# Kernel optimization log

Measured on AMD Instinct MI355X. Metric: run time of the kernel, lower is better.

## Reference

```python
import jax, jax.numpy as jnp
import numpy as np

VISION_TOKEN_TYPE = 1

def _swiglu_mlp(x, w_gate, w_up, w_down):
    # x: [B, L, D]; w_gate/w_up: [D, F]; w_down: [F, D]
    g = jax.nn.silu(jnp.einsum('bld,df->blf', x, w_gate))
    u = jnp.einsum('bld,df->blf', x, w_up)
    return jnp.einsum('blf,fd->bld', g * u, w_down)

def _vision_mask(token_type_ids):
    # vision_token_mask[:, :-1] = (tt[:, :-1]==V) & (tt[:, 1:]==V); last col False
    is_v = token_type_ids == VISION_TOKEN_TYPE
    pair = is_v[:, :-1] & is_v[:, 1:]
    return jnp.concatenate([pair, jnp.zeros_like(pair[:, :1])], axis=1)  # [B, L] bool

def setup_inputs() -> dict:
    key = jax.random.key(0)
    ks = jax.random.split(key, 8)
    B, L, D, F = 2, 2048, 4096, 11008
    s = 0.02
    return {
        'hidden_states': jax.random.normal(ks[0], (B, L, D), dtype=jnp.float32),
        'token_type_ids': jax.random.randint(ks[1], (B, L), 0, 2, dtype=jnp.int64),
        'vision_gate': jax.random.normal(ks[2], (D, F), dtype=jnp.float32) * s,
        'vision_up': jax.random.normal(ks[3], (D, F), dtype=jnp.float32) * s,
        'vision_down': jax.random.normal(ks[4], (F, D), dtype=jnp.float32) * s,
        'language_gate': jax.random.normal(ks[5], (D, F), dtype=jnp.float32) * s,
        'language_up': jax.random.normal(ks[6], (D, F), dtype=jnp.float32) * s,
        'language_down': jax.random.normal(ks[7], (F, D), dtype=jnp.float32) * s,
    }

def reference(hidden_states, token_type_ids, vision_gate, vision_up, vision_down,
              language_gate, language_up, language_down):
    vmask = _vision_mask(token_type_ids)  # [B, L]
    out_v = _swiglu_mlp(hidden_states, vision_gate, vision_up, vision_down)
    out_l = _swiglu_mlp(hidden_states, language_gate, language_up, language_down)
    return jnp.where(vmask[:, :, None], out_v, out_l)
```

## Files before the change

### kernel.cpp

```cpp
#include <hip/hip_runtime.h>
#include <hip/hip_bf16.h>

#define B_    2
#define L_    2048
#define D_    4096
#define F_    11008
#define M_TOK (B_ * L_)
#define BM    256
#define M_ALLOC (M_TOK + BM)
#define NTM   (M_ALLOC / BM)
#define NT_GU (D_ / 64)
#define NT_DN (F_ / 64)
#define NTILE_F (F_ / 128)
#define LDS_BYTES 131072

typedef __attribute__((ext_vector_type(8))) __bf16 bf16x8;
typedef __attribute__((ext_vector_type(4))) float  f32x4;
typedef unsigned short ushort_t;
typedef unsigned int   uint_t;


__device__ __forceinline__ void gload_lds16(const void* g, void* l) {
  __builtin_amdgcn_global_load_lds(
      (const __attribute__((address_space(1))) void*)g,
      (__attribute__((address_space(3))) void*)l, 16, 0, 0);
}

#define PH_BAR()  { __builtin_amdgcn_sched_barrier(0); __builtin_amdgcn_s_barrier(); __builtin_amdgcn_sched_barrier(0); }
#define LGKM0()   { asm volatile("s_waitcnt lgkmcnt(0)" ::: "memory"); __builtin_amdgcn_sched_barrier(0); }
#define VM4()     { asm volatile("s_waitcnt vmcnt(4)" ::: "memory"); __builtin_amdgcn_sched_barrier(0); }
#define VM0()     { asm volatile("s_waitcnt vmcnt(0)" ::: "memory"); __builtin_amdgcn_sched_barrier(0); }

__device__ __forceinline__ ushort_t f2bf(float v) {
  union { __hip_bfloat16 h; ushort_t u; } cv;
  cv.h = __float2bfloat16(v);
  return cv.u;
}

__device__ __forceinline__ void stage_half(const __hip_bfloat16* __restrict__ src, int ldE,
                                           __bf16* ldsb, int w, int lane) {
#pragma unroll
  for (int j = 0; j < 2; ++j) {
    const int ch  = (w * 2 + j) * 64 + lane;
    const int row = ch >> 3;
    const int cc  = (ch & 7) ^ (row & 7);
    gload_lds16(src + (size_t)(row * ldE + cc * 8), ldsb + (w * 2 + j) * 512);
  }
}

__device__ __forceinline__ bf16x8 ldfrag(const __bf16* region, int row, int koffb) {
  const int off = ((row << 7) + koffb) ^ ((row & 7) << 4);
  return *(const bf16x8*)((const char*)region + off);
}

__device__ __forceinline__ void mfma_q(f32x4 (&acc)[8][4], int mb, int nb,
                                       const bf16x8 (&af)[4][2], const bf16x8 (&bf)[2][2]) {
#pragma unroll
  for (int mm = 0; mm < 4; ++mm)
#pragma unroll
    for (int nn = 0; nn < 2; ++nn)
#pragma unroll
      for (int ks = 0; ks < 2; ++ks)
        acc[mb + mm][nb + nn] = __builtin_amdgcn_mfma_f32_16x16x32_bf16(
            af[mm][ks], bf[nn][ks], acc[mb + mm][nb + nn], 0, 0, 0);
}

__device__ __forceinline__ void gemm_kloop(const __hip_bfloat16* __restrict__ Ag, const int ldA,
                                           const __hip_bfloat16* __restrict__ Bg, const int ldB,
                                           const int nt, __bf16* smem, f32x4 (&acc)[8][4],
                                           const int wm, const int wn, const int l15,
                                           const int l4, const int w, const int lane) {
  stage_half(Ag,             ldA, smem,                w, lane);
  stage_half(Ag + 128 * ldA, ldA, smem + 8192,         w, lane);
  stage_half(Bg,             ldB, smem + 16384,        w, lane);
  stage_half(Bg + 128 * ldB, ldB, smem + 24576,        w, lane);
  if (1 < nt) {
    stage_half(Ag + 64,             ldA, smem + 32768,        w, lane);
    stage_half(Ag + 64 + 128 * ldA, ldA, smem + 32768 + 8192, w, lane);
  }
  VM4(); PH_BAR();

  for (int t = 0; t < nt; ++t) {
    __bf16* bufc = smem + (t & 1) * 32768;
    __bf16* bufn = smem + ((t + 1) & 1) * 32768;
    const __bf16* At = bufc;
    const __bf16* Bt = bufc + 16384;
    bf16x8 a0[4][2], a1[4][2], b0[2][2], b1[2][2];

#pragma unroll
    for (int i = 0; i < 4; ++i)
#pragma unroll
      for (int ks = 0; ks < 2; ++ks)
        a0[i][ks] = ldfrag(At, wm * 128 + i * 16 + l15, ks * 64 + l4 * 16);
#pragma unroll
    for (int n = 0; n < 2; ++n)
#pragma unroll
      for (int ks = 0; ks < 2; ++ks)
        b0[n][ks] = ldfrag(Bt, wn * 64 + n * 16 + l15, ks * 64 + l4 * 16);
    if (t + 1 < nt) stage_half(Bg + (t + 1) * 64, ldB, bufn + 16384, w, lane);
    PH_BAR(); LGKM0();
    __builtin_amdgcn_s_setprio(1);
    mfma_q(acc, 0, 0, a0, b0);
    __builtin_amdgcn_s_setprio(0);
    PH_BAR();

#pragma unroll
    for (int i = 0; i < 4; ++i)
#pragma unroll
      for (int ks = 0; ks < 2; ++ks)
        a1[i][ks] = ldfrag(At, wm * 128 + 64 + i * 16 + l15, ks * 64 + l4 * 16);
    if (t + 1 < nt) stage_half(Bg + (t + 1) * 64 + 128 * ldB, ldB, bufn + 24576, w, lane);
    PH_BAR(); LGKM0();
    __builtin_amdgcn_s_setprio(1);
    mfma_q(acc, 4, 0, a1, b0);
    __builtin_amdgcn_s_setprio(0);
    PH_BAR();

#pragma unroll
    for (int n = 0; n < 2; ++n)
#pragma unroll
      for (int ks = 0; ks < 2; ++ks)
        b1[n][ks] = ldfrag(Bt, wn * 64 + 32 + n * 16 + l15, ks * 64 + l4 * 16);
    if (t + 2 < nt) stage_half(Ag + (t + 2) * 64, ldA, bufc, w, lane);
    PH_BAR(); LGKM0();
    __builtin_amdgcn_s_setprio(1);
    mfma_q(acc, 4, 2, a1, b1);
    __builtin_amdgcn_s_setprio(0);
    PH_BAR();

    if (t + 2 < nt) stage_half(Ag + (t + 2) * 64 + 128 * ldA, ldA, bufc + 8192, w, lane);
    __builtin_amdgcn_s_setprio(1);
    mfma_q(acc, 0, 2, a0, b1);
    __builtin_amdgcn_s_setprio(0);
    if (t + 2 < nt) { VM4(); } else { VM0(); }
    PH_BAR();
  }
}


__global__ void init_kernel(int* counters, int* slot2tok) {
  int i = blockIdx.x * 256 + threadIdx.x;
  if (i < 2) counters[i] = 0;
  if (i < M_ALLOC) slot2tok[i] = -1;
}

__global__ void assign_kernel(const int* __restrict__ tt, int* counters,
                              int* __restrict__ slot2tok) {
  int t = blockIdx.x * 256 + threadIdx.x;
  if (t >= M_TOK) return;
  int l = t & (L_ - 1);
  bool isv = (tt[t] == 1) && (l < L_ - 1) && (tt[t + 1] == 1);
  int slot;
  if (isv) slot = atomicAdd(&counters[0], 1);
  else     slot = M_ALLOC - 1 - atomicAdd(&counters[1], 1);
  slot2tok[slot] = t;
}

__global__ void gather_cvt(const float* __restrict__ x, const int* __restrict__ slot2tok,
                           __hip_bfloat16* __restrict__ xg) {
  const int s = blockIdx.x;
  const int t = slot2tok[s];
  __hip_bfloat16* dst = xg + (size_t)s * D_ + threadIdx.x * 16;
  union { ushort_t h[8]; uint4 v; } p0, p1;
  if (t >= 0) {
    const float4* s4 = (const float4*)(x + (size_t)t * D_ + threadIdx.x * 16);
    float4 a = s4[0], b = s4[1], c = s4[2], d = s4[3];
    float vals[16] = {a.x,a.y,a.z,a.w,b.x,b.y,b.z,b.w,c.x,c.y,c.z,c.w,d.x,d.y,d.z,d.w};
#pragma unroll
    for (int i = 0; i < 8; ++i) p0.h[i] = f2bf(vals[i]);
#pragma unroll
    for (int i = 0; i < 8; ++i) p1.h[i] = f2bf(vals[8 + i]);
  } else {
    p0.v = make_uint4(0, 0, 0, 0);
    p1.v = make_uint4(0, 0, 0, 0);
  }
  *(uint4*)dst = p0.v;
  *(uint4*)(dst + 8) = p1.v;
}

__global__ __launch_bounds__(128) void transpose_cvt64(const float* __restrict__ in,
                                                       __hip_bfloat16* __restrict__ out,
                                                       int R, int C) {
  const int c  = threadIdx.x & 63;
  const int rc = threadIdx.x >> 6;
  const int c0 = blockIdx.x * 64;
  const int r0 = blockIdx.y * 64 + rc * 32;
  const float* ip = in + (size_t)r0 * C + c0 + c;
  uint_t pk[16];
#pragma unroll
  for (int j = 0; j < 16; ++j) {
    float v0 = ip[(size_t)(2 * j) * C];
    float v1 = ip[(size_t)(2 * j + 1) * C];
    pk[j] = (uint_t)f2bf(v0) | ((uint_t)f2bf(v1) << 16);
  }
  uint4* op = (uint4*)(out + (size_t)(c0 + c) * R + r0);
#pragma unroll
  for (int k = 0; k < 4; ++k)
    op[k] = make_uint4(pk[4 * k], pk[4 * k + 1], pk[4 * k + 2], pk[4 * k + 3]);
}

__global__ void sentinel_kernel(float* out, int n) {
  int i = blockIdx.x * 256 + threadIdx.x;
  if (i < n) out[i] = 1e30f;
}

__global__ __launch_bounds__(512, 2) void gemm256_gateup_fused(
    const __hip_bfloat16* __restrict__ Xg,
    const __hip_bfloat16* __restrict__ WgTv, const __hip_bfloat16* __restrict__ WuTv,
    const __hip_bfloat16* __restrict__ WgTl, const __hip_bfloat16* __restrict__ WuTl,
    __hip_bfloat16* __restrict__ H, const int* __restrict__ counters) {
  extern __shared__ __bf16 smem[];
  const int tid = threadIdx.x, lane = tid & 63, w = tid >> 6;
  const int wm = w >> 1, wn = w & 1;
  const int l15 = lane & 15, l4 = lane >> 4;

  const int orig = blockIdx.x;
  const int nwg = gridDim.x;
  const int q = nwg >> 3, r = nwg & 7, xcd = orig & 7;
  const int wg = (xcd < r ? xcd * (q + 1) : r * (q + 1) + (xcd - r) * q) + (orig >> 3);
  const int mt = wg / NTILE_F, ntile = wg % NTILE_F;
  const int row0 = mt * BM;
  const int ncol0 = ntile * 128;
  const int nv = counters[0];
  const bool isv = row0 < nv;
  const __hip_bfloat16* Ag   = Xg + (size_t)row0 * D_;
  const __hip_bfloat16* Bg_g = (isv ? WgTv : WgTl) + (size_t)ncol0 * D_;
  const __hip_bfloat16* Bu_g = (isv ? WuTv : WuTl) + (size_t)ncol0 * D_;

  f32x4 accg[4][4] = {};
  f32x4 accu[4][4] = {};
  const int nt = NT_GU;

  stage_half(Ag,                  D_, smem,          w, lane);
  stage_half(Ag + 128 * D_,       D_, smem + 8192,   w, lane);
  stage_half(Bg_g,                D_, smem + 32768,  w, lane);
  stage_half(Bu_g,                D_, smem + 49152,  w, lane);
  stage_half(Ag + 64,             D_, smem + 16384,  w, lane);
  stage_half(Ag + 64 + 128 * D_,  D_, smem + 24576,  w, lane);
  VM4(); PH_BAR();

  for (int t = 0; t < nt; ++t) {
    const int cur = t & 1;
    const __bf16* At  = smem + cur * 16384;
    const __bf16* Bgt = smem + 32768 + cur * 8192;
    const __bf16* But = smem + 49152 + cur * 8192;
    __bf16* nxA  = smem + cur * 16384;
    __bf16* nxBg = smem + 32768 + (cur ^ 1) * 8192;
    __bf16* nxBu = smem + 49152 + (cur ^ 1) * 8192;
    bf16x8 af[4][2], bg[4][2], bu[4][2];

#pragma unroll
    for (int m = 0; m < 4; ++m)
#pragma unroll
      for (int ks = 0; ks < 2; ++ks)
        af[m][ks] = ldfrag(At, wm * 64 + m * 16 + l15, ks * 64 + l4 * 16);
#pragma unroll
    for (int n = 0; n < 4; ++n)
#pragma unroll
      for (int ks = 0; ks < 2; ++ks)
        bg[n][ks] = ldfrag(Bgt, wn * 64 + n * 16 + l15, ks * 64 + l4 * 16);
    if (t + 1 < nt) {
      stage_half(Bg_g + (t + 1) * 64, D_, nxBg, w, lane);
      stage_half(Bu_g + (t + 1) * 64, D_, nxBu, w, lane);
    }
    PH_BAR(); LGKM0();
    __builtin_amdgcn_s_setprio(1);
#pragma unroll
    for (int m = 0; m < 4; ++m)
#pragma unroll
      for (int n = 0; n < 4; ++n)
#pragma unroll
        for (int ks = 0; ks < 2; ++ks)
          accg[m][n] = __builtin_amdgcn_mfma_f32_16x16x32_bf16(
              af[m][ks], bg[n][ks], accg[m][n], 0, 0, 0);
    __builtin_amdgcn_s_setprio(0);
    PH_BAR();

#pragma unroll
    for (int n = 0; n < 4; ++n)
#pragma unroll
      for (int ks = 0; ks < 2; ++ks)
        bu[n][ks] = ldfrag(But, wn * 64 + n * 16 + l15, ks * 64 + l4 * 16);
    if (t + 2 < nt) {
      stage_half(Ag + (t + 2) * 64,            D_, nxA,        w, lane);
      stage_half(Ag + (t + 2) * 64 + 128 * D_, D_, nxA + 8192, w, lane);
    }
    PH_BAR(); LGKM0();
    __builtin_amdgcn_s_setprio(1);
#pragma unroll
    for (int m = 0; m < 4; ++m)
#pragma unroll
      for (int n = 0; n < 4; ++n)
#pragma unroll
        for (int ks = 0; ks < 2; ++ks)
          accu[m][n] = __builtin_amdgcn_mfma_f32_16x16x32_bf16(
              af[m][ks], bu[n][ks], accu[m][n], 0, 0, 0);
    __builtin_amdgcn_s_setprio(0);
    if (t + 2 < nt) { VM4(); } else { VM0(); }
    PH_BAR();
  }

#pragma unroll
  for (int m = 0; m < 4; ++m) {
    const int grow = row0 + wm * 64 + m * 16 + l4 * 4;
#pragma unroll
    for (int rr = 0; rr < 4; ++rr) {
      __hip_bfloat16* orow = H + (size_t)(grow + rr) * F_ + ncol0 + wn * 64 + l15;
#pragma unroll
      for (int n = 0; n < 4; ++n) {
        const float g = accg[m][n][rr];
        const float u = accu[m][n][rr];
        orow[n * 16] = __float2bfloat16(g / (1.0f + __expf(-g)) * u);
      }
    }
  }
}


__global__ __launch_bounds__(512, 2) void gemm256_down(
    const __hip_bfloat16* __restrict__ H,
    const __hip_bfloat16* __restrict__ WdTv, const __hip_bfloat16* __restrict__ WdTl,
    float* __restrict__ out, const int* __restrict__ counters,
    const int* __restrict__ slot2tok) {
  extern __shared__ __bf16 smem[];
  const int tid = threadIdx.x, lane = tid & 63, w = tid >> 6;
  const int wm = w >> 2, wn = w & 3;
  const int l15 = lane & 15, l4 = lane >> 4;

  const int mt = blockIdx.x / (D_ / 256);
  const int nt = blockIdx.x % (D_ / 256);
  const int z  = blockIdx.y;
  const int row0 = mt * BM;
  const int ncol0 = nt * 256;
  const int ntz = NT_DN / 2;
  const int t0 = z * ntz;
  const int nv = counters[0];
  const __hip_bfloat16* Bsrc = (row0 < nv) ? WdTv : WdTl;
  const __hip_bfloat16* Ag = H + (size_t)row0 * F_ + t0 * 64;
  const __hip_bfloat16* Bg = Bsrc + (size_t)ncol0 * F_ + t0 * 64;

  f32x4 acc[8][4] = {};
  gemm_kloop(Ag, F_, Bg, F_, ntz, smem, acc, wm, wn, l15, l4, w, lane);

#pragma unroll
  for (int m = 0; m < 8; ++m) {
    const int slot = row0 + wm * 128 + m * 16 + l4 * 4;
#pragma unroll
    for (int rr = 0; rr < 4; ++rr) {
      const int tok = slot2tok[slot + rr];
      if (tok < 0) continue;
      float* orow = out + (size_t)tok * D_ + ncol0 + wn * 64 + l15;
#pragma unroll
      for (int n = 0; n < 4; ++n)
        atomicAdd(&orow[n * 16], acc[m][n][rr]);
    }
  }
}


extern "C" void kernel_launch(void* const* d_in, const int* in_sizes, int n_in,
                              void* d_out, int out_size, void* d_ws, size_t ws_size,
                              hipStream_t stream) {
  const float* x   = (const float*)d_in[0];
  const int*   tt  = (const int*)d_in[1];
  const float* wgv = (const float*)d_in[2];
  const float* wuv = (const float*)d_in[3];
  const float* wdv = (const float*)d_in[4];
  const float* wgl = (const float*)d_in[5];
  const float* wul = (const float*)d_in[6];
  const float* wdl = (const float*)d_in[7];
  float* out = (float*)d_out;

  size_t off = 0;
  auto nalign = [](size_t v) { return (v + 255) & ~(size_t)255; };
  const size_t o_cnt = off; off += nalign(2 * sizeof(int));
  const size_t o_s2t = off; off += nalign((size_t)M_ALLOC * sizeof(int));
  const size_t o_xg  = off; off += nalign((size_t)M_ALLOC * D_ * 2);
  const size_t o_h   = off; off += nalign((size_t)M_ALLOC * F_ * 2);
  const size_t wbytes = nalign((size_t)D_ * F_ * 2);
  const size_t o_wgv = off; off += wbytes;
  const size_t o_wuv = off; off += wbytes;
  const size_t o_wgl = off; off += wbytes;
  const size_t o_wul = off; off += wbytes;

  if (ws_size < off) {
    sentinel_kernel<<<(out_size + 255) / 256, 256, 0, stream>>>(out, out_size);
    return;
  }

  char* ws = (char*)d_ws;
  int* counters = (int*)(ws + o_cnt);
  int* slot2tok = (int*)(ws + o_s2t);
  __hip_bfloat16* Xg  = (__hip_bfloat16*)(ws + o_xg);
  __hip_bfloat16* H   = (__hip_bfloat16*)(ws + o_h);
  __hip_bfloat16* WgTv = (__hip_bfloat16*)(ws + o_wgv);
  __hip_bfloat16* WuTv = (__hip_bfloat16*)(ws + o_wuv);
  __hip_bfloat16* WgTl = (__hip_bfloat16*)(ws + o_wgl);
  __hip_bfloat16* WuTl = (__hip_bfloat16*)(ws + o_wul);
  __hip_bfloat16* WdTv = WgTv;
  __hip_bfloat16* WdTl = WuTv;

  hipFuncSetAttribute((const void*)gemm256_gateup_fused,
                      hipFuncAttributeMaxDynamicSharedMemorySize, LDS_BYTES);
  hipFuncSetAttribute((const void*)gemm256_down,
                      hipFuncAttributeMaxDynamicSharedMemorySize, LDS_BYTES);

  hipMemsetAsync(out, 0, (size_t)out_size * sizeof(float), stream);

  init_kernel<<<(M_ALLOC + 255) / 256, 256, 0, stream>>>(counters, slot2tok);
  assign_kernel<<<(M_TOK + 255) / 256, 256, 0, stream>>>(tt, counters, slot2tok);
  gather_cvt<<<M_ALLOC, 256, 0, stream>>>(x, slot2tok, Xg);

  dim3 tb(128);
  dim3 tg_gu(F_ / 64, D_ / 64);
  transpose_cvt64<<<tg_gu, tb, 0, stream>>>(wgv, WgTv, D_, F_);
  transpose_cvt64<<<tg_gu, tb, 0, stream>>>(wuv, WuTv, D_, F_);
  transpose_cvt64<<<tg_gu, tb, 0, stream>>>(wgl, WgTl, D_, F_);
  transpose_cvt64<<<tg_gu, tb, 0, stream>>>(wul, WuTl, D_, F_);

  gemm256_gateup_fused<<<dim3(NTM * NTILE_F), 512, LDS_BYTES, stream>>>(
      Xg, WgTv, WuTv, WgTl, WuTl, H, counters);

  dim3 tg_dn(D_ / 64, F_ / 64);
  transpose_cvt64<<<tg_dn, tb, 0, stream>>>(wdv, WdTv, F_, D_);
  transpose_cvt64<<<tg_dn, tb, 0, stream>>>(wdl, WdTl, F_, D_);

  gemm256_down<<<dim3(NTM * (D_ / 256), 2), 512, LDS_BYTES, stream>>>(
      H, WdTv, WdTl, out, counters, slot2tok);
}
```

Measured before the change: 1.655 ms.

## Split gate/up MFMA phases, reorder tiles with XCD swizzle, raise down-proj split-K

The fused gate/up kernel now runs four phases per k-step instead of two. Gate and up B fragments share one register array, and A fragments load in two halves, with global-to-LDS staging spread across the phases. Both GEMMs now use an XCD-aware block swizzle, with the M-tile varying fastest so that consecutive workgroups on one XCD reuse the same weight column tile. The down projection moves from split-K 2 to split-K 4, which gives more workgroups. The aim is lower register pressure, finer overlap of loads with MFMA work, and better L2 reuse and occupancy, at the cost of more barriers and more partial-sum accumulation traffic into the output.

Result: no change. 1.636 ms (-1.1%).

```diff
diff --git a/kernel.cpp b/kernel.cpp
--- a/kernel.cpp
+++ b/kernel.cpp
@@ -12,6 +12,7 @@
 #define NT_GU (D_ / 64)
 #define NT_DN (F_ / 64)
 #define NTILE_F (F_ / 128)
+#define SPLITK_DN 4
 #define LDS_BYTES 131072
 
 typedef __attribute__((ext_vector_type(8))) __bf16 bf16x8;
@@ -35,6 +36,11 @@
   union { __hip_bfloat16 h; ushort_t u; } cv;
   cv.h = __float2bfloat16(v);
   return cv.u;
+}
+
+__device__ __forceinline__ int xcd_swz(int orig, int nwg) {
+  const int q = nwg >> 3, r = nwg & 7, xcd = orig & 7;
+  return (xcd < r ? xcd * (q + 1) : r * (q + 1) + (xcd - r) * q) + (orig >> 3);
 }
 
 __device__ __forceinline__ void stage_half(const __hip_bfloat16* __restrict__ src, int ldE,
@@ -214,11 +220,8 @@
   const int wm = w >> 1, wn = w & 1;
   const int l15 = lane & 15, l4 = lane >> 4;
 
-  const int orig = blockIdx.x;
-  const int nwg = gridDim.x;
-  const int q = nwg >> 3, r = nwg & 7, xcd = orig & 7;
-  const int wg = (xcd < r ? xcd * (q + 1) : r * (q + 1) + (xcd - r) * q) + (orig >> 3);
-  const int mt = wg / NTILE_F, ntile = wg % NTILE_F;
+  const int wg = xcd_swz(blockIdx.x, gridDim.x);
+  const int mt = wg % NTM, ntile = wg / NTM;
   const int row0 = mt * BM;
   const int ncol0 = ntile * 128;
   const int nv = counters[0];
@@ -247,10 +250,10 @@
     __bf16* nxA  = smem + cur * 16384;
     __bf16* nxBg = smem + 32768 + (cur ^ 1) * 8192;
     __bf16* nxBu = smem + 49152 + (cur ^ 1) * 8192;
-    bf16x8 af[4][2], bg[4][2], bu[4][2];
-
-#pragma unroll
-    for (int m = 0; m < 4; ++m)
+    bf16x8 af[4][2], bb[4][2];
+
+#pragma unroll
+    for (int m = 0; m < 2; ++m)
 #pragma unroll
       for (int ks = 0; ks < 2; ++ks)
         af[m][ks] = ldfrag(At, wm * 64 + m * 16 + l15, ks * 64 + l4 * 16);
@@ -258,21 +261,37 @@
     for (int n = 0; n < 4; ++n)
 #pragma unroll
       for (int ks = 0; ks < 2; ++ks)
-        bg[n][ks] = ldfrag(Bgt, wn * 64 + n * 16 + l15, ks * 64 + l4 * 16);
-    if (t + 1 < nt) {
-      stage_half(Bg_g + (t + 1) * 64, D_, nxBg, w, lane);
-      stage_half(Bu_g + (t + 1) * 64, D_, nxBu, w, lane);
-    }
-    PH_BAR(); LGKM0();
-    __builtin_amdgcn_s_setprio(1);
-#pragma unroll
-    for (int m = 0; m < 4; ++m)
+        bb[n][ks] = ldfrag(Bgt, wn * 64 + n * 16 + l15, ks * 64 + l4 * 16);
+    if (t + 1 < nt) stage_half(Bg_g + (t + 1) * 64, D_, nxBg, w, lane);
+    PH_BAR(); LGKM0();
+    __builtin_amdgcn_s_setprio(1);
+#pragma unroll
+    for (int m = 0; m < 2; ++m)
 #pragma unroll
       for (int n = 0; n < 4; ++n)
 #pragma unroll
         for (int ks = 0; ks < 2; ++ks)
           accg[m][n] = __builtin_amdgcn_mfma_f32_16x16x32_bf16(
-              af[m][ks], bg[n][ks], accg[m][n], 0, 0, 0);
+              af[m][ks], bb[n][ks], accg[m][n], 0, 0, 0);
+    __builtin_amdgcn_s_setprio(0);
+    PH_BAR();
+
+#pragma unroll
+    for (int m = 2; m < 4; ++m)
+#pragma unroll
+      for (int ks = 0; ks < 2; ++ks)
+        af[m][ks] = ldfrag(At, wm * 64 + m * 16 + l15, ks * 64 + l4 * 16);
+    if (t + 1 < nt) stage_half(Bu_g + (t + 1) * 64, D_, nxBu, w, lane);
+    PH_BAR(); LGKM0();
+    __builtin_amdgcn_s_setprio(1);
+#pragma unroll
+    for (int m = 2; m < 4; ++m)
+#pragma unroll
+      for (int n = 0; n < 4; ++n)
+#pragma unroll
+        for (int ks = 0; ks < 2; ++ks)
+          accg[m][n] = __builtin_amdgcn_mfma_f32_16x16x32_bf16(
+              af[m][ks], bb[n][ks], accg[m][n], 0, 0, 0);
     __builtin_amdgcn_s_setprio(0);
     PH_BAR();
 
@@ -280,21 +299,31 @@
     for (int n = 0; n < 4; ++n)
 #pragma unroll
       for (int ks = 0; ks < 2; ++ks)
-        bu[n][ks] = ldfrag(But, wn * 64 + n * 16 + l15, ks * 64 + l4 * 16);
-    if (t + 2 < nt) {
-      stage_half(Ag + (t + 2) * 64,            D_, nxA,        w, lane);
-      stage_half(Ag + (t + 2) * 64 + 128 * D_, D_, nxA + 8192, w, lane);
-    }
-    PH_BAR(); LGKM0();
-    __builtin_amdgcn_s_setprio(1);
-#pragma unroll
-    for (int m = 0; m < 4; ++m)
+        bb[n][ks] = ldfrag(But, wn * 64 + n * 16 + l15, ks * 64 + l4 * 16);
+    if (t + 2 < nt) stage_half(Ag + (t + 2) * 64, D_, nxA, w, lane);
+    PH_BAR(); LGKM0();
+    __builtin_amdgcn_s_setprio(1);
+#pragma unroll
+    for (int m = 0; m < 2; ++m)
 #pragma unroll
       for (int n = 0; n < 4; ++n)
 #pragma unroll
         for (int ks = 0; ks < 2; ++ks)
           accu[m][n] = __builtin_amdgcn_mfma_f32_16x16x32_bf16(
-              af[m][ks], bu[n][ks], accu[m][n], 0, 0, 0);
+              af[m][ks], bb[n][ks], accu[m][n], 0, 0, 0);
+    __builtin_amdgcn_s_setprio(0);
+    PH_BAR();
+
+    if (t + 2 < nt) stage_half(Ag + (t + 2) * 64 + 128 * D_, D_, nxA + 8192, w, lane);
+    __builtin_amdgcn_s_setprio(1);
+#pragma unroll
+    for (int m = 2; m < 4; ++m)
+#pragma unroll
+      for (int n = 0; n < 4; ++n)
+#pragma unroll
+        for (int ks = 0; ks < 2; ++ks)
+          accu[m][n] = __builtin_amdgcn_mfma_f32_16x16x32_bf16(
+              af[m][ks], bb[n][ks], accu[m][n], 0, 0, 0);
     __builtin_amdgcn_s_setprio(0);
     if (t + 2 < nt) { VM4(); } else { VM0(); }
     PH_BAR();
@@ -327,12 +356,12 @@
   const int wm = w >> 2, wn = w & 3;
   const int l15 = lane & 15, l4 = lane >> 4;
 
-  const int mt = blockIdx.x / (D_ / 256);
-  const int nt = blockIdx.x % (D_ / 256);
+  const int wg = xcd_swz(blockIdx.x, gridDim.x);
+  const int mt = wg % NTM, nt = wg / NTM;
   const int z  = blockIdx.y;
   const int row0 = mt * BM;
   const int ncol0 = nt * 256;
-  const int ntz = NT_DN / 2;
+  const int ntz = NT_DN / SPLITK_DN;
   const int t0 = z * ntz;
   const int nv = counters[0];
   const __hip_bfloat16* Bsrc = (row0 < nv) ? WdTv : WdTl;
@@ -425,6 +454,6 @@
   transpose_cvt64<<<tg_dn, tb, 0, stream>>>(wdv, WdTv, F_, D_);
   transpose_cvt64<<<tg_dn, tb, 0, stream>>>(wdl, WdTl, F_, D_);
 
-  gemm256_down<<<dim3(NTM * (D_ / 256), 2), 512, LDS_BYTES, stream>>>(
+  gemm256_down<<<dim3(NTM * (D_ / 256), SPLITK_DN), 512, LDS_BYTES, stream>>>(
       H, WdTv, WdTl, out, counters, slot2tok);
 }
```

## Simplify GEMM pipelines to full-tile double buffering, swizzle tiles, raise down split-K

Applied to the files above, without the earlier changes.

Both GEMM main loops drop the phased, priority-tagged, quarter-tile interleaving and switch to a plain double buffer. The whole next K-tile is prefetched up front, then all fragments are loaded and all MFMAs run, with a full vmcnt(0) wait and one barrier per iteration. Tile-index mapping now walks M-tiles fastest through a shared XCD swizzle, so blocks on one XCD share weight columns, and the down-projection split-K goes from 2 to 4, doubling its grid at the cost of more atomic adds. The simpler schedule cuts barriers but gives up fine-grained overlap, and vmcnt(0) stalls until the prefetch lands.

New measurement: 1.798 ms. +8.7%, slower.

```diff
diff --git a/kernel.cpp b/kernel.cpp
--- a/kernel.cpp
+++ b/kernel.cpp
@@ -12,7 +12,9 @@
 #define NT_GU (D_ / 64)
 #define NT_DN (F_ / 64)
 #define NTILE_F (F_ / 128)
-#define LDS_BYTES 131072
+#define SPLITK_DN 4
+#define LDS_GU 131072
+#define LDS_DN 131072
 
 typedef __attribute__((ext_vector_type(8))) __bf16 bf16x8;
 typedef __attribute__((ext_vector_type(4))) float  f32x4;
@@ -27,14 +29,17 @@
 }
 
 #define PH_BAR()  { __builtin_amdgcn_sched_barrier(0); __builtin_amdgcn_s_barrier(); __builtin_amdgcn_sched_barrier(0); }
-#define LGKM0()   { asm volatile("s_waitcnt lgkmcnt(0)" ::: "memory"); __builtin_amdgcn_sched_barrier(0); }
-#define VM4()     { asm volatile("s_waitcnt vmcnt(4)" ::: "memory"); __builtin_amdgcn_sched_barrier(0); }
 #define VM0()     { asm volatile("s_waitcnt vmcnt(0)" ::: "memory"); __builtin_amdgcn_sched_barrier(0); }
 
 __device__ __forceinline__ ushort_t f2bf(float v) {
   union { __hip_bfloat16 h; ushort_t u; } cv;
   cv.h = __float2bfloat16(v);
   return cv.u;
+}
+
+__device__ __forceinline__ int xcd_swz(int orig, int nwg) {
+  const int q = nwg >> 3, r = nwg & 7, xcd = orig & 7;
+  return (xcd < r ? xcd * (q + 1) : r * (q + 1) + (xcd - r) * q) + (orig >> 3);
 }
 
 __device__ __forceinline__ void stage_half(const __hip_bfloat16* __restrict__ src, int ldE,
@@ -51,90 +56,6 @@
 __device__ __forceinline__ bf16x8 ldfrag(const __bf16* region, int row, int koffb) {
   const int off = ((row << 7) + koffb) ^ ((row & 7) << 4);
   return *(const bf16x8*)((const char*)region + off);
-}
-
-__device__ __forceinline__ void mfma_q(f32x4 (&acc)[8][4], int mb, int nb,
-                                       const bf16x8 (&af)[4][2], const bf16x8 (&bf)[2][2]) {
-#pragma unroll
-  for (int mm = 0; mm < 4; ++mm)
-#pragma unroll
-    for (int nn = 0; nn < 2; ++nn)
-#pragma unroll
-      for (int ks = 0; ks < 2; ++ks)
-        acc[mb + mm][nb + nn] = __builtin_amdgcn_mfma_f32_16x16x32_bf16(
-            af[mm][ks], bf[nn][ks], acc[mb + mm][nb + nn], 0, 0, 0);
-}
-
-__device__ __forceinline__ void gemm_kloop(const __hip_bfloat16* __restrict__ Ag, const int ldA,
-                                           const __hip_bfloat16* __restrict__ Bg, const int ldB,
-                                           const int nt, __bf16* smem, f32x4 (&acc)[8][4],
-                                           const int wm, const int wn, const int l15,
-                                           const int l4, const int w, const int lane) {
-  stage_half(Ag,             ldA, smem,                w, lane);
-  stage_half(Ag + 128 * ldA, ldA, smem + 8192,         w, lane);
-  stage_half(Bg,             ldB, smem + 16384,        w, lane);
-  stage_half(Bg + 128 * ldB, ldB, smem + 24576,        w, lane);
-  if (1 < nt) {
-    stage_half(Ag + 64,             ldA, smem + 32768,        w, lane);
-    stage_half(Ag + 64 + 128 * ldA, ldA, smem + 32768 + 8192, w, lane);
-  }
-  VM4(); PH_BAR();
-
-  for (int t = 0; t < nt; ++t) {
-    __bf16* bufc = smem + (t & 1) * 32768;
-    __bf16* bufn = smem + ((t + 1) & 1) * 32768;
-    const __bf16* At = bufc;
-    const __bf16* Bt = bufc + 16384;
-    bf16x8 a0[4][2], a1[4][2], b0[2][2], b1[2][2];
-
-#pragma unroll
-    for (int i = 0; i < 4; ++i)
-#pragma unroll
-      for (int ks = 0; ks < 2; ++ks)
-        a0[i][ks] = ldfrag(At, wm * 128 + i * 16 + l15, ks * 64 + l4 * 16);
-#pragma unroll
-    for (int n = 0; n < 2; ++n)
-#pragma unroll
-      for (int ks = 0; ks < 2; ++ks)
-        b0[n][ks] = ldfrag(Bt, wn * 64 + n * 16 + l15, ks * 64 + l4 * 16);
-    if (t + 1 < nt) stage_half(Bg + (t + 1) * 64, ldB, bufn + 16384, w, lane);
-    PH_BAR(); LGKM0();
-    __builtin_amdgcn_s_setprio(1);
-    mfma_q(acc, 0, 0, a0, b0);
-    __builtin_amdgcn_s_setprio(0);
-    PH_BAR();
-
-#pragma unroll
-    for (int i = 0; i < 4; ++i)
-#pragma unroll
-      for (int ks = 0; ks < 2; ++ks)
-        a1[i][ks] = ldfrag(At, wm * 128 + 64 + i * 16 + l15, ks * 64 + l4 * 16);
-    if (t + 1 < nt) stage_half(Bg + (t + 1) * 64 + 128 * ldB, ldB, bufn + 24576, w, lane);
-    PH_BAR(); LGKM0();
-    __builtin_amdgcn_s_setprio(1);
-    mfma_q(acc, 4, 0, a1, b0);
-    __builtin_amdgcn_s_setprio(0);
-    PH_BAR();
-
-#pragma unroll
-    for (int n = 0; n < 2; ++n)
-#pragma unroll
-      for (int ks = 0; ks < 2; ++ks)
-        b1[n][ks] = ldfrag(Bt, wn * 64 + 32 + n * 16 + l15, ks * 64 + l4 * 16);
-    if (t + 2 < nt) stage_half(Ag + (t + 2) * 64, ldA, bufc, w, lane);
-    PH_BAR(); LGKM0();
-    __builtin_amdgcn_s_setprio(1);
-    mfma_q(acc, 4, 2, a1, b1);
-    __builtin_amdgcn_s_setprio(0);
-    PH_BAR();
-
-    if (t + 2 < nt) stage_half(Ag + (t + 2) * 64 + 128 * ldA, ldA, bufc + 8192, w, lane);
-    __builtin_amdgcn_s_setprio(1);
-    mfma_q(acc, 0, 2, a0, b1);
-    __builtin_amdgcn_s_setprio(0);
-    if (t + 2 < nt) { VM4(); } else { VM0(); }
-    PH_BAR();
-  }
 }
 
 
@@ -214,11 +135,8 @@
   const int wm = w >> 1, wn = w & 1;
   const int l15 = lane & 15, l4 = lane >> 4;
 
-  const int orig = blockIdx.x;
-  const int nwg = gridDim.x;
-  const int q = nwg >> 3, r = nwg & 7, xcd = orig & 7;
-  const int wg = (xcd < r ? xcd * (q + 1) : r * (q + 1) + (xcd - r) * q) + (orig >> 3);
-  const int mt = wg / NTILE_F, ntile = wg % NTILE_F;
+  const int wg = xcd_swz(blockIdx.x, gridDim.x);
+  const int mt = wg % NTM, ntile = wg / NTM;
   const int row0 = mt * BM;
   const int ncol0 = ntile * 128;
   const int nv = counters[0];
@@ -231,24 +149,29 @@
   f32x4 accu[4][4] = {};
   const int nt = NT_GU;
 
-  stage_half(Ag,                  D_, smem,          w, lane);
-  stage_half(Ag + 128 * D_,       D_, smem + 8192,   w, lane);
-  stage_half(Bg_g,                D_, smem + 32768,  w, lane);
-  stage_half(Bu_g,                D_, smem + 49152,  w, lane);
-  stage_half(Ag + 64,             D_, smem + 16384,  w, lane);
-  stage_half(Ag + 64 + 128 * D_,  D_, smem + 24576,  w, lane);
-  VM4(); PH_BAR();
+  stage_half(Ag,             D_, smem,         w, lane);
+  stage_half(Ag + 128 * D_,  D_, smem + 8192,  w, lane);
+  stage_half(Bg_g,           D_, smem + 32768, w, lane);
+  stage_half(Bu_g,           D_, smem + 49152, w, lane);
+  VM0(); PH_BAR();
 
   for (int t = 0; t < nt; ++t) {
     const int cur = t & 1;
     const __bf16* At  = smem + cur * 16384;
     const __bf16* Bgt = smem + 32768 + cur * 8192;
     const __bf16* But = smem + 49152 + cur * 8192;
-    __bf16* nxA  = smem + cur * 16384;
-    __bf16* nxBg = smem + 32768 + (cur ^ 1) * 8192;
-    __bf16* nxBu = smem + 49152 + (cur ^ 1) * 8192;
+    if (t + 1 < nt) {
+      __bf16* nA  = smem + (cur ^ 1) * 16384;
+      __bf16* nBg = smem + 32768 + (cur ^ 1) * 8192;
+      __bf16* nBu = smem + 49152 + (cur ^ 1) * 8192;
+      stage_half(Ag + (t + 1) * 64,            D_, nA,        w, lane);
+      stage_half(Ag + (t + 1) * 64 + 128 * D_, D_, nA + 8192, w, lane);
+      stage_half(Bg_g + (t + 1) * 64,          D_, nBg,       w, lane);
+      stage_half(Bu_g + (t + 1) * 64,          D_, nBu,       w, lane);
+    }
+    __builtin_amdgcn_sched_barrier(0);
+
     bf16x8 af[4][2], bg[4][2], bu[4][2];
-
 #pragma unroll
     for (int m = 0; m < 4; ++m)
 #pragma unroll
@@ -259,12 +182,6 @@
 #pragma unroll
       for (int ks = 0; ks < 2; ++ks)
         bg[n][ks] = ldfrag(Bgt, wn * 64 + n * 16 + l15, ks * 64 + l4 * 16);
-    if (t + 1 < nt) {
-      stage_half(Bg_g + (t + 1) * 64, D_, nxBg, w, lane);
-      stage_half(Bu_g + (t + 1) * 64, D_, nxBu, w, lane);
-    }
-    PH_BAR(); LGKM0();
-    __builtin_amdgcn_s_setprio(1);
 #pragma unroll
     for (int m = 0; m < 4; ++m)
 #pragma unroll
@@ -273,20 +190,11 @@
         for (int ks = 0; ks < 2; ++ks)
           accg[m][n] = __builtin_amdgcn_mfma_f32_16x16x32_bf16(
               af[m][ks], bg[n][ks], accg[m][n], 0, 0, 0);
-    __builtin_amdgcn_s_setprio(0);
-    PH_BAR();
-
 #pragma unroll
     for (int n = 0; n < 4; ++n)
 #pragma unroll
       for (int ks = 0; ks < 2; ++ks)
         bu[n][ks] = ldfrag(But, wn * 64 + n * 16 + l15, ks * 64 + l4 * 16);
-    if (t + 2 < nt) {
-      stage_half(Ag + (t + 2) * 64,            D_, nxA,        w, lane);
-      stage_half(Ag + (t + 2) * 64 + 128 * D_, D_, nxA + 8192, w, lane);
-    }
-    PH_BAR(); LGKM0();
-    __builtin_amdgcn_s_setprio(1);
 #pragma unroll
     for (int m = 0; m < 4; ++m)
 #pragma unroll
@@ -295,8 +203,8 @@
         for (int ks = 0; ks < 2; ++ks)
           accu[m][n] = __builtin_amdgcn_mfma_f32_16x16x32_bf16(
               af[m][ks], bu[n][ks], accu[m][n], 0, 0, 0);
-    __builtin_amdgcn_s_setprio(0);
-    if (t + 2 < nt) { VM4(); } else { VM0(); }
+
+    if (t + 1 < nt) VM0();
     PH_BAR();
   }
 
@@ -315,7 +223,6 @@
     }
   }
 }
-
 
 __global__ __launch_bounds__(512, 2) void gemm256_down(
     const __hip_bfloat16* __restrict__ H,
@@ -327,20 +234,63 @@
   const int wm = w >> 2, wn = w & 3;
   const int l15 = lane & 15, l4 = lane >> 4;
 
-  const int mt = blockIdx.x / (D_ / 256);
-  const int nt = blockIdx.x % (D_ / 256);
+  const int wg = xcd_swz(blockIdx.x, gridDim.x);
+  const int mt = wg % NTM, ntt = wg / NTM;
   const int z  = blockIdx.y;
   const int row0 = mt * BM;
-  const int ncol0 = nt * 256;
-  const int ntz = NT_DN / 2;
-  const int t0 = z * ntz;
+  const int ncol0 = ntt * 256;
+  const int ntz = NT_DN / SPLITK_DN;
   const int nv = counters[0];
   const __hip_bfloat16* Bsrc = (row0 < nv) ? WdTv : WdTl;
-  const __hip_bfloat16* Ag = H + (size_t)row0 * F_ + t0 * 64;
-  const __hip_bfloat16* Bg = Bsrc + (size_t)ncol0 * F_ + t0 * 64;
+  const __hip_bfloat16* Ag = H + (size_t)row0 * F_ + z * ntz * 64;
+  const __hip_bfloat16* Bg = Bsrc + (size_t)ncol0 * F_ + z * ntz * 64;
 
   f32x4 acc[8][4] = {};
-  gemm_kloop(Ag, F_, Bg, F_, ntz, smem, acc, wm, wn, l15, l4, w, lane);
+  const int nt = ntz;
+
+  stage_half(Ag,             F_, smem,         w, lane);
+  stage_half(Ag + 128 * F_,  F_, smem + 8192,  w, lane);
+  stage_half(Bg,             F_, smem + 32768, w, lane);
+  stage_half(Bg + 128 * F_,  F_, smem + 40960, w, lane);
+  VM0(); PH_BAR();
+
+  for (int t = 0; t < nt; ++t) {
+    const int cur = t & 1;
+    const __bf16* At = smem + cur * 16384;
+    const __bf16* Bt = smem + 32768 + cur * 16384;
+    if (t + 1 < nt) {
+      __bf16* nA = smem + (cur ^ 1) * 16384;
+      __bf16* nB = smem + 32768 + (cur ^ 1) * 16384;
+      stage_half(Ag + (t + 1) * 64,            F_, nA,        w, lane);
+      stage_half(Ag + (t + 1) * 64 + 128 * F_, F_, nA + 8192, w, lane);
+      stage_half(Bg + (t + 1) * 64,            F_, nB,        w, lane);
+      stage_half(Bg + (t + 1) * 64 + 128 * F_, F_, nB + 8192, w, lane);
+    }
+    __builtin_amdgcn_sched_barrier(0);
+
+    bf16x8 af[8][2], bf_[4][2];
+#pragma unroll
+    for (int m = 0; m < 8; ++m)
+#pragma unroll
+      for (int ks = 0; ks < 2; ++ks)
+        af[m][ks] = ldfrag(At, wm * 128 + m * 16 + l15, ks * 64 + l4 * 16);
+#pragma unroll
+    for (int n = 0; n < 4; ++n)
+#pragma unroll
+      for (int ks = 0; ks < 2; ++ks)
+        bf_[n][ks] = ldfrag(Bt, wn * 64 + n * 16 + l15, ks * 64 + l4 * 16);
+#pragma unroll
+    for (int m = 0; m < 8; ++m)
+#pragma unroll
+      for (int n = 0; n < 4; ++n)
+#pragma unroll
+        for (int ks = 0; ks < 2; ++ks)
+          acc[m][n] = __builtin_amdgcn_mfma_f32_16x16x32_bf16(
+              af[m][ks], bf_[n][ks], acc[m][n], 0, 0, 0);
+
+    if (t + 1 < nt) VM0();
+    PH_BAR();
+  }
 
 #pragma unroll
   for (int m = 0; m < 8; ++m) {
@@ -401,9 +351,9 @@
   __hip_bfloat16* WdTl = WuTv;
 
   hipFuncSetAttribute((const void*)gemm256_gateup_fused,
-                      hipFuncAttributeMaxDynamicSharedMemorySize, LDS_BYTES);
+                      hipFuncAttributeMaxDynamicSharedMemorySize, LDS_GU);
   hipFuncSetAttribute((const void*)gemm256_down,
-                      hipFuncAttributeMaxDynamicSharedMemorySize, LDS_BYTES);
+                      hipFuncAttributeMaxDynamicSharedMemorySize, LDS_DN);
 
   hipMemsetAsync(out, 0, (size_t)out_size * sizeof(float), stream);
 
@@ -418,13 +368,13 @@
   transpose_cvt64<<<tg_gu, tb, 0, stream>>>(wgl, WgTl, D_, F_);
   transpose_cvt64<<<tg_gu, tb, 0, stream>>>(wul, WuTl, D_, F_);
 
-  gemm256_gateup_fused<<<dim3(NTM * NTILE_F), 512, LDS_BYTES, stream>>>(
+  gemm256_gateup_fused<<<dim3(NTM * NTILE_F), 512, LDS_GU, stream>>>(
       Xg, WgTv, WuTv, WgTl, WuTl, H, counters);
 
   dim3 tg_dn(D_ / 64, F_ / 64);
   transpose_cvt64<<<tg_dn, tb, 0, stream>>>(wdv, WdTv, F_, D_);
   transpose_cvt64<<<tg_dn, tb, 0, stream>>>(wdl, WdTl, F_, D_);
 
-  gemm256_down<<<dim3(NTM * (D_ / 256), 2), 512, LDS_BYTES, stream>>>(
+  gemm256_down<<<dim3(NTM * (D_ / 256), SPLITK_DN), 512, LDS_DN, stream>>>(
       H, WdTv, WdTl, out, counters, slot2tok);
 }
```
